# Kernel optimization log

Measured on AMD Instinct MI355X. Metric: run time of the kernel, lower is better.

## Reference

```python
import jax, jax.numpy as jnp
import numpy as np
from jax import lax

B, C, H, W = 4, 128, 256, 256
HEADS = 8
HIDDEN = int(C * 2)  # ffn_expansion_factor=2
THETA = 0.7


def _p(key, shape, scale=0.05):
    return jax.random.normal(key, shape, dtype=jnp.float32) * scale


def setup_inputs() -> dict:
    key = jax.random.key(0)
    ks = jax.random.split(key, 32)
    inp = {
        'ms': jax.random.normal(ks[0], (B, C, H, W), dtype=jnp.float32),
        'pan': jax.random.normal(ks[1], (B, C, H, W), dtype=jnp.float32),
        # LayerNorms (WithBias)
        'ln1_w': jnp.ones((C,), jnp.float32),
        'ln1_b': jnp.zeros((C,), jnp.float32),
        'ln2_w': jnp.ones((2 * C,), jnp.float32),
        'ln2_b': jnp.zeros((2 * C,), jnp.float32),
        # Attention (bias=False)
        'qkv_w': _p(ks[2], (C, C)),            # 1x1 conv weight [out,in]
        'dw_w': _p(ks[3], (C, 1, 3, 3)),       # depthwise 3x3 (Conv2d_cd)
        'temperature': jnp.ones((HEADS, 1, 1), jnp.float32),
        'proj_w': _p(ks[4], (C, C)),
        # Freprocess (default bias=True)
        'pre1_w': _p(ks[5], (C, C)), 'pre1_b': jnp.zeros((C,), jnp.float32),
        'pre2_w': _p(ks[6], (C, C)), 'pre2_b': jnp.zeros((C,), jnp.float32),
        'amp1_w': _p(ks[7], (C, 2 * C)), 'amp1_b': jnp.zeros((C,), jnp.float32),
        'amp2_w': _p(ks[8], (C, C)), 'amp2_b': jnp.zeros((C,), jnp.float32),
        'pha1_w': _p(ks[9], (C, 2 * C)), 'pha1_b': jnp.zeros((C,), jnp.float32),
        'pha2_w': _p(ks[10], (C, C)), 'pha2_b': jnp.zeros((C,), jnp.float32),
        'post_w': _p(ks[11], (C, C)), 'post_b': jnp.zeros((C,), jnp.float32),
        # FFN (bias=False)
        'pin_w': _p(ks[12], (2 * HIDDEN, 2 * C)),
        'pout_w': _p(ks[13], (C, HIDDEN)),
    }
    return inp


def conv1x1(x, w, b=None):
    y = jnp.einsum('bchw,oc->bohw', x, w)
    if b is not None:
        y = y + b[None, :, None, None]
    return y


def layernorm_c(x, w, b):
    # per-pixel LayerNorm over channel dim (torch var unbiased=False, eps=1e-5)
    mu = jnp.mean(x, axis=1, keepdims=True)
    var = jnp.mean((x - mu) ** 2, axis=1, keepdims=True)
    return (x - mu) / jnp.sqrt(var + 1e-5) * w[None, :, None, None] + b[None, :, None, None]


def dwconv_cd(x, w):
    # central-difference depthwise conv: dw3x3(x) - theta * (sum(kernel) * x)
    y = lax.conv_general_dilated(x, w, (1, 1), ((1, 1), (1, 1)),
                                 dimension_numbers=('NCHW', 'OIHW', 'NCHW'),
                                 feature_group_count=x.shape[1])
    ksum = w.sum(axis=(1, 2, 3))  # (C,)
    return y - THETA * x * ksum[None, :, None, None]


def attention(nms, npan, qkv_w, dw_w, temperature, proj_w):
    b, c, h, w = nms.shape
    ch = c // HEADS
    q = dwconv_cd(conv1x1(nms, qkv_w), dw_w)
    kv = dwconv_cd(conv1x1(npan, qkv_w), dw_w)  # k == v in source
    q = q.reshape(b, HEADS, ch, h * w)
    k = kv.reshape(b, HEADS, ch, h * w)
    v = k
    q = q / jnp.maximum(jnp.linalg.norm(q, axis=-1, keepdims=True), 1e-12)
    k = k / jnp.maximum(jnp.linalg.norm(k, axis=-1, keepdims=True), 1e-12)
    attn = jnp.einsum('bhcn,bhdn->bhcd', q, k) * temperature[None]
    attn = jax.nn.softmax(attn, axis=-1)
    out = jnp.einsum('bhcd,bhdn->bhcn', attn, v).reshape(b, c, h, w)
    return conv1x1(out, proj_w)


def freprocess(msf, panf, pre1_w, pre1_b, pre2_w, pre2_b,
               amp1_w, amp1_b, amp2_w, amp2_b,
               pha1_w, pha1_b, pha2_w, pha2_b, post_w, post_b):
    h, w = msf.shape[-2:]
    msF = jnp.fft.rfft2(conv1x1(msf, pre1_w, pre1_b) + 1e-8)
    panF = jnp.fft.rfft2(conv1x1(panf, pre2_w, pre2_b) + 1e-8)
    amp_in = jnp.concatenate([jnp.abs(msF), jnp.abs(panF)], axis=1)
    pha_in = jnp.concatenate([jnp.angle(msF), jnp.angle(panF)], axis=1)
    amp = conv1x1(jax.nn.leaky_relu(conv1x1(amp_in, amp1_w, amp1_b), 0.1), amp2_w, amp2_b)
    pha = conv1x1(jax.nn.leaky_relu(conv1x1(pha_in, pha1_w, pha1_b), 0.1), pha2_w, pha2_b)
    real = amp * jnp.cos(pha) + 1e-8
    imag = amp * jnp.sin(pha) + 1e-8
    out = jax.lax.complex(real, imag) + 1e-8
    out = jnp.abs(jnp.fft.irfft2(out, s=(h, w)))
    return conv1x1(out, post_w, post_b)


def ffn(x, pin_w, pout_w):
    y = conv1x1(x, pin_w)
    x1, x2 = jnp.split(y, 2, axis=1)
    return conv1x1(jax.nn.gelu(x1, approximate=False) * x2, pout_w)


def reference(ms, pan, ln1_w, ln1_b, ln2_w, ln2_b, qkv_w, dw_w, temperature,
              proj_w, pre1_w, pre1_b, pre2_w, pre2_b, amp1_w, amp1_b, amp2_w,
              amp2_b, pha1_w, pha1_b, pha2_w, pha2_b, post_w, post_b,
              pin_w, pout_w):
    x = ms + attention(layernorm_c(ms, ln1_w, ln1_b),
                       layernorm_c(pan, ln1_w, ln1_b),
                       qkv_w, dw_w, temperature, proj_w)
    frefuse = freprocess(ms, pan, pre1_w, pre1_b, pre2_w, pre2_b,
                         amp1_w, amp1_b, amp2_w, amp2_b,
                         pha1_w, pha1_b, pha2_w, pha2_b, post_w, post_b)
    frespa = jnp.concatenate([x, frefuse], axis=1)
    x = x + ffn(layernorm_c(frespa, ln2_w, ln2_b), pin_w, pout_w)
    return x
```

## Files before the change

kernel.cpp:

```cpp
#include <hip/hip_runtime.h>
#include <math.h>

#define B_ 4
#define C_ 128
#define HW_ 65536
#define H__ 256
#define KF_ 129
#define PLANEF_ 33024

typedef __attribute__((ext_vector_type(8))) short short8v;
typedef __attribute__((ext_vector_type(4))) float f32x4;
typedef __attribute__((ext_vector_type(4))) unsigned short ush4;
typedef __attribute__((ext_vector_type(8))) unsigned short ush8;
typedef __attribute__((ext_vector_type(4))) unsigned uint4v;

__device__ __forceinline__ unsigned short f2bf(float f) {
    union { float f; unsigned u; } v; v.f = f;
    return (unsigned short)((v.u + 0x7FFFu + ((v.u >> 16) & 1u)) >> 16);
}
__device__ __forceinline__ float bf2f(unsigned short s) {
    union { unsigned u; float f; } v; v.u = (unsigned)s << 16;
    return v.f;
}
__device__ __forceinline__ unsigned pack2bf(float2 v) {
// ... 109 lines not shown
{
    __shared__ unsigned short xs[128][136];
    __shared__ float2 lnred[LNF ? 8 : 1][LNF ? 128 : 1];
    __shared__ float2 lnmi[LNF ? 128 : 1];
    const int t = threadIdx.x;
    const int bz = blockIdx.z;
    const int p0 = blockIdx.x * 128;
    const int lane = t & 63;
    const int wr = t >> 7, wc = (t >> 6) & 1;
    const int lr = lane >> 4, lc = lane & 15;

    if constexpr (INBF == 0) {
        const float* Xb = (const float*)Xv + (size_t)bz * sx;
        const int px4 = t & 31;
        float s0 = 0.f, s1 = 0.f, s2v = 0.f, s3 = 0.f;
        float q0 = 0.f, q1 = 0.f, q2 = 0.f, q3 = 0.f;
#pragma unroll
        for (int g = 0; g < 2; ++g) {
            float4 st[8];
#pragma unroll
            for (int i = 0; i < 8; ++i) {
                int e = t + (g * 8 + i) * 256;
                int c = e >> 5;
                st[i] = *(const float4*)(Xb + (size_t)c * plane + p0 + px4 * 4);
            }
#pragma unroll
            for (int i = 0; i < 8; ++i) {
                int e = t + (g * 8 + i) * 256;
                int c = e >> 5;
                float a0 = st[i].x, a1 = st[i].y, a2 = st[i].z, a3 = st[i].w;
                if constexpr (PRO == 1) {
                    a0 = a0 > 0.f ? a0 : 0.1f * a0;
                    a1 = a1 > 0.f ? a1 : 0.1f * a1;
                    a2 = a2 > 0.f ? a2 : 0.1f * a2;
                    a3 = a3 > 0.f ? a3 : 0.1f * a3;
                }
                if constexpr (LNF) {
                    s0 += a0; q0 += a0 * a0;
                    s1 += a1; q1 += a1 * a1;
                    s2v += a2; q2 += a2 * a2;
                    s3 += a3; q3 += a3 * a3;
                }
                *(unsigned short*)swz_ptr(xs, px4 * 4 + 0, 2 * c) = f2bf(a0);
                *(unsigned short*)swz_ptr(xs, px4 * 4 + 1, 2 * c) = f2bf(a1);
                *(unsigned short*)swz_ptr(xs, px4 * 4 + 2, 2 * c) = f2bf(a2);
                *(unsigned short*)swz_ptr(xs, px4 * 4 + 3, 2 * c) = f2bf(a3);
            }
        }
        if constexpr (LNF) {
            lnred[t >> 5][px4 * 4 + 0] = make_float2(s0, q0);
            lnred[t >> 5][px4 * 4 + 1] = make_float2(s1, q1);
            lnred[t >> 5][px4 * 4 + 2] = make_float2(s2v, q2);
            lnred[t >> 5][px4 * 4 + 3] = make_float2(s3, q3);
        }
    } else {
        const unsigned short* Xb = (const unsigned short*)Xv + (size_t)bz * sx;
        ush8 st[8];
#pragma unroll
        for (int i = 0; i < 8; ++i) {
            int e = t + i * 256;
            int c = e >> 4, px8 = e & 15;
            st[i] = *(const ush8*)(Xb + (size_t)c * plane + p0 + px8 * 8);
        }
#pragma unroll
        for (int i = 0; i < 8; ++i) {
            int e = t + i * 256;
            int c = e >> 4, px8 = e & 15;
#pragma unroll
            for (int j = 0; j < 8; ++j) {
                unsigned short us = (unsigned short)st[i][j];
                if constexpr (PRO == 1) {
                    float f = bf2f(us);
                    f = f > 0.f ? f : 0.1f * f;
                    us = f2bf(f);
                }
                *(unsigned short*)swz_ptr(xs, px8 * 8 + j, 2 * c) = us;
            }
        }
    }
    __syncthreads();
    if constexpr (LNF) {
        if (t < 128) {
            float ss = 0.f, qq = 0.f;
#pragma unroll
            for (int j = 0; j < 8; ++j) { float2 a = lnred[j][t]; ss += a.x; qq += a.y; }
            float m = ss * (1.f / 128.f);
            float inv = rsqrtf(qq * (1.f / 128.f) - m * m + 1e-5f);
            lnmi[t] = make_float2(m, inv);
        }
        __syncthreads();
    }

    f32x4 acc[4][4];
#pragma unroll
    for (int mi = 0; mi < 4; ++mi)
#pragma unroll
        for (int ni = 0; ni < 4; ++ni) acc[mi][ni] = (f32x4){0.f, 0.f, 0.f, 0.f};

#pragma unroll
    for (int kk = 0; kk < 128; kk += 32) {
        short8v bfr[4];
#pragma unroll
        for (int ni = 0; ni < 4; ++ni)
            bfr[ni] = *(const short8v*)swz_ptr(xs, wc * 64 + ni * 16 + lc, 2 * (kk + lr * 8));
#pragma unroll
        for (int mi = 0; mi < 4; ++mi) {
            int row = wr * 64 + mi * 16 + lc;
            short8v afr = *(const short8v*)(Wb + (size_t)row * wstride + kk + lr * 8);
#pragma unroll
            for (int ni = 0; ni < 4; ++ni)
                acc[mi][ni] = __builtin_amdgcn_mfma_f32_16x16x32_bf16(afr, bfr[ni], acc[mi][ni], 0, 0, 0);
        }
    }

    float2 mrow[4];
    if constexpr (LNF) {
#pragma unroll
        for (int ni = 0; ni < 4; ++ni) mrow[ni] = lnmi[wc * 64 + ni * 16 + lc];
    }

#pragma unroll
    for (int mi = 0; mi < 4; ++mi) {
        int ob = wr * 64 + mi * 16 + lr * 4;
#pragma unroll
        for (int r = 0; r < 4; ++r) {
            int o = ob + r;
            float bv = 0.f, wso = 0.f;
            if constexpr (LNF) { bv = bsum[o]; wso = wsum[o]; }
            else { if (bias) bv = bias[o]; if (flags & 1) bv += 1e-8f; }
#pragma unroll
            for (int ni = 0; ni < 4; ++ni) {
                int px = wc * 64 + ni * 16 + lc;
                float v;
                if constexpr (LNF) {
                    float m = mrow[ni].x, inv = mrow[ni].y;
                    v = acc[mi][ni][r] * inv + bv - m * inv * wso;
                } else {
                    v = acc[mi][ni][r] + bv;
                }
                if constexpr (OUTBF == 0) {
                    float* Y = (float*)Yv;
                    size_t yi = (size_t)bz * sy + (size_t)o * plane + p0 + px;
                    if (res) v += res[(size_t)bz * sres + (size_t)o * plane + p0 + px];
                    Y[yi] = v;
                } else {
                    unsigned short* Y = (unsigned short*)Yv;
                    Y[(size_t)bz * sy + (size_t)o * plane + p0 + px] = f2bf(v);
                }
            }
        }
    }
}

__global__ __launch_bounds__(256, 2) void apconv2(
    const unsigned* __restrict__ T1, const unsigned* __restrict__ T2, size_t sT,
    const unsigned short* __restrict__ Wa1, const unsigned short* __restrict__ Wp1,
    const unsigned short* __restrict__ Wa2, const unsigned short* __restrict__ Wp2,
    const float* __restrict__ ba1, const float* __restrict__ bp1,
    const float* __restrict__ ba2, const float* __restrict__ bp2,
    unsigned short* __restrict__ AMP, unsigned short* __restrict__ PHA, size_t sO)
{
    __shared__ __align__(16) unsigned short buf[2][128][72];
    const int t = threadIdx.x;
    const int bz = blockIdx.z;
    const int p0 = blockIdx.x * 128;
    const int lane = t & 63;
    const int wr = t >> 7, wc = (t >> 6) & 1;
    const int lr = lane >> 4, lc = lane & 15;
    const int px2 = t & 63;

    typedef unsigned short (*row72)[72];
    typedef unsigned short (*row144)[144];
    row72 xa = (row72)buf[0];
    row72 xp = (row72)buf[1];
    row144 hb = (row144)&buf[0][0][0];

    f32x4 aa[4][4], ap[4][4];
#pragma unroll
    for (int mi = 0; mi < 4; ++mi)
#pragma unroll
        for (int ni = 0; ni < 4; ++ni) { aa[mi][ni] = (f32x4){0.f,0.f,0.f,0.f}; ap[mi][ni] = (f32x4){0.f,0.f,0.f,0.f}; }

    for (int ch = 0; ch < 256; ch += 64) {
        const unsigned* Ts = ((ch < 128) ? T1 : T2) + (size_t)bz * sT + (size_t)(ch & 127) * PLANEF_;
#pragma unroll
        for (int g = 0; g < 2; ++g) {
            uint2 st[8];
#pragma unroll
            for (int i = 0; i < 8; ++i) {
                int e = t + (g * 8 + i) * 256;
                int c = e >> 6;
                st[i] = *(const uint2*)(Ts + (size_t)c * PLANEF_ + p0 + px2 * 2);
            }
#pragma unroll
            for (int i = 0; i < 8; ++i) {
                int e = t + (g * 8 + i) * 256;
                int c = e >> 6;
                float2 z0 = upk(st[i].x), z1 = upk(st[i].y);
                float m0 = sqrtf(z0.x * z0.x + z0.y * z0.y);
                float m1 = sqrtf(z1.x * z1.x + z1.y * z1.y);
                float a0 = fatan2(z0.y, z0.x);
                float a1 = fatan2(z1.y, z1.x);
                *(unsigned short*)swz_ptr(xa, px2 * 2 + 0, 2 * c) = f2bf(m0);
                *(unsigned short*)swz_ptr(xa, px2 * 2 + 1, 2 * c) = f2bf(m1);
                *(unsigned short*)swz_ptr(xp, px2 * 2 + 0, 2 * c) = f2bf(a0);
                *(unsigned short*)swz_ptr(xp, px2 * 2 + 1, 2 * c) = f2bf(a1);
            }
        }
        __syncthreads();
#pragma unroll
        for (int kk = 0; kk < 64; kk += 32) {
            short8v bfa[4], bfp[4];
#pragma unroll
            for (int ni = 0; ni < 4; ++ni) {
                bfa[ni] = *(const short8v*)swz_ptr(xa, wc * 64 + ni * 16 + lc, 2 * (kk + lr * 8));
                bfp[ni] = *(const short8v*)swz_ptr(xp, wc * 64 + ni * 16 + lc, 2 * (kk + lr * 8));
            }
#pragma unroll
            for (int mi = 0; mi < 4; ++mi) {
                int row = wr * 64 + mi * 16 + lc;
                short8v afa = *(const short8v*)(Wa1 + (size_t)row * 256 + ch + kk + lr * 8);
                short8v afp = *(const short8v*)(Wp1 + (size_t)row * 256 + ch + kk + lr * 8);
#pragma unroll
                for (int ni = 0; ni < 4; ++ni) {
                    aa[mi][ni] = __builtin_amdgcn_mfma_f32_16x16x32_bf16(afa, bfa[ni], aa[mi][ni], 0, 0, 0);
                    ap[mi][ni] = __builtin_amdgcn_mfma_f32_16x16x32_bf16(afp, bfp[ni], ap[mi][ni], 0, 0, 0);
                }
            }
        }
        __syncthreads();
    }

#pragma unroll
    for (int mi = 0; mi < 4; ++mi)
#pragma unroll
        for (int r = 0; r < 4; ++r) {
            int o = wr * 64 + mi * 16 + lr * 4 + r;
            float bva = ba1[o];
#pragma unroll
            for (int ni = 0; ni < 4; ++ni) {
                int px = wc * 64 + ni * 16 + lc;
                float v = aa[mi][ni][r] + bva;
                v = v > 0.f ? v : 0.1f * v;
                *(unsigned short*)swz_ptr(hb, px, 2 * o) = f2bf(v);
            }
        }
    __syncthreads();
    {
        f32x4 acc[4][4];
#pragma unroll
        for (int mi = 0; mi < 4; ++mi)
#pragma unroll
            for (int ni = 0; ni < 4; ++ni) acc[mi][ni] = (f32x4){0.f,0.f,0.f,0.f};
#pragma unroll
        for (int kk = 0; kk < 128; kk += 32) {
            short8v bfr[4];
#pragma unroll
            for (int ni = 0; ni < 4; ++ni)
                bfr[ni] = *(const short8v*)swz_ptr(hb, wc * 64 + ni * 16 + lc, 2 * (kk + lr * 8));
#pragma unroll
            for (int mi = 0; mi < 4; ++mi) {
                int row = wr * 64 + mi * 16 + lc;
                short8v afr = *(const short8v*)(Wa2 + (size_t)row * 128 + kk + lr * 8);
#pragma unroll
                for (int ni = 0; ni < 4; ++ni)
                    acc[mi][ni] = __builtin_amdgcn_mfma_f32_16x16x32_bf16(afr, bfr[ni], acc[mi][ni], 0, 0, 0);
            }
        }
#pragma unroll
        for (int mi = 0; mi < 4; ++mi)
#pragma unroll
            for (int r = 0; r < 4; ++r) {
                int o = wr * 64 + mi * 16 + lr * 4 + r;
                float bv = ba2[o];
#pragma unroll
                for (int ni = 0; ni < 4; ++ni) {
                    int px = wc * 64 + ni * 16 + lc;
                    AMP[(size_t)bz * sO + (size_t)o * PLANEF_ + p0 + px] = f2bf(acc[mi][ni][r] + bv);
                }
            }
    }
    __syncthreads();

#pragma unroll
    for (int mi = 0; mi < 4; ++mi)
#pragma unroll
        for (int r = 0; r < 4; ++r) {
            int o = wr * 64 + mi * 16 + lr * 4 + r;
            float bvp = bp1[o];
#pragma unroll
            for (int ni = 0; ni < 4; ++ni) {
                int px = wc * 64 + ni * 16 + lc;
                float v = ap[mi][ni][r] + bvp;
                v = v > 0.f ? v : 0.1f * v;
                *(unsigned short*)swz_ptr(hb, px, 2 * o) = f2bf(v);
            }
        }
    __syncthreads();
    {
        f32x4 acc[4][4];
#pragma unroll
        for (int mi = 0; mi < 4; ++mi)
#pragma unroll
            for (int ni = 0; ni < 4; ++ni) acc[mi][ni] = (f32x4){0.f,0.f,0.f,0.f};
#pragma unroll
        for (int kk = 0; kk < 128; kk += 32) {
            short8v bfr[4];
#pragma unroll
            for (int ni = 0; ni < 4; ++ni)
                bfr[ni] = *(const short8v*)swz_ptr(hb, wc * 64 + ni * 16 + lc, 2 * (kk + lr * 8));
#pragma unroll
            for (int mi = 0; mi < 4; ++mi) {
                int row = wr * 64 + mi * 16 + lc;
                short8v afr = *(const short8v*)(Wp2 + (size_t)row * 128 + kk + lr * 8);
#pragma unroll
                for (int ni = 0; ni < 4; ++ni)
                    acc[mi][ni] = __builtin_amdgcn_mfma_f32_16x16x32_bf16(afr, bfr[ni], acc[mi][ni], 0, 0, 0);
            }
        }
#pragma unroll
        for (int mi = 0; mi < 4; ++mi)
#pragma unroll
            for (int r = 0; r < 4; ++r) {
                int o = wr * 64 + mi * 16 + lr * 4 + r;
                float bv = bp2[o];
#pragma unroll
                for (int ni = 0; ni < 4; ++ni) {
                    int px = wc * 64 + ni * 16 + lc;
                    PHA[(size_t)bz * sO + (size_t)o * PLANEF_ + p0 + px] = f2bf(acc[mi][ni][r] + bv);
                }
            }
    }
}

__global__ __launch_bounds__(256, 3) void ffn_mfma6(
    const float* __restrict__ x, const unsigned short* __restrict__ fre,
    const unsigned short* __restrict__ pinb,
    const unsigned short* __restrict__ pout2,
    const float4* __restrict__ pinC,
    float* __restrict__ out)
{
    __shared__ unsigned short xs[64][264];
    __shared__ unsigned short hs[64][136];
    __shared__ float2 muinv[64];
    float2* sred = (float2*)&hs[0][0];
    const int b = blockIdx.y;
    const size_t p0 = (size_t)blockIdx.x * 64;
    const int t = threadIdx.x;
    const int wave = t >> 6, lane = t & 63;
    const int lr = lane >> 4, lc = lane & 15;
    const int px4 = t & 15;

    float s0 = 0.f, s1 = 0.f, s2v = 0.f, s3 = 0.f;
    float q0 = 0.f, q1 = 0.f, q2 = 0.f, q3 = 0.f;
    {
        float4 stx[8];
        ush4 stf[8];
#pragma unroll
        for (int i = 0; i < 8; ++i) {
            int e = t + i * 256;
            int c = e >> 4;
            stx[i] = *(const float4*)(x + ((size_t)b * 128 + c) * HW_ + p0 + px4 * 4);
        }
#pragma unroll
        for (int i = 0; i < 8; ++i) {
            int e = t + i * 256;
            int c = e >> 4;
            stf[i] = *(const ush4*)(fre + (size_t)b * 8388608 + (size_t)c * HW_ + p0 + px4 * 4);
        }
#pragma unroll
        for (int i = 0; i < 8; ++i) {
            int e = t + i * 256;
            int c = e >> 4;
            float a0 = stx[i].x, a1 = stx[i].y, a2 = stx[i].z, a3 = stx[i].w;
            s0 += a0; q0 += a0 * a0;
            s1 += a1; q1 += a1 * a1;
            s2v += a2; q2 += a2 * a2;
            s3 += a3; q3 += a3 * a3;
            *(unsigned short*)swz_ptr(xs, px4 * 4 + 0, 2 * c) = f2bf(a0);
            *(unsigned short*)swz_ptr(xs, px4 * 4 + 1, 2 * c) = f2bf(a1);
            *(unsigned short*)swz_ptr(xs, px4 * 4 + 2, 2 * c) = f2bf(a2);
            *(unsigned short*)swz_ptr(xs, px4 * 4 + 3, 2 * c) = f2bf(a3);
        }
#pragma unroll
        for (int i = 0; i < 8; ++i) {
            int e = t + i * 256;
            int c = e >> 4;
            float a0 = bf2f((unsigned short)stf[i][0]);
            float a1 = bf2f((unsigned short)stf[i][1]);
            float a2 = bf2f((unsigned short)stf[i][2]);
            float a3 = bf2f((unsigned short)stf[i][3]);
            s0 += a0; q0 += a0 * a0;
            s1 += a1; q1 += a1 * a1;
            s2v += a2; q2 += a2 * a2;
            s3 += a3; q3 += a3 * a3;
            *(unsigned short*)swz_ptr(xs, px4 * 4 + 0, 2 * (128 + c)) = (unsigned short)stf[i][0];
            *(unsigned short*)swz_ptr(xs, px4 * 4 + 1, 2 * (128 + c)) = (unsigned short)stf[i][1];
            *(unsigned short*)swz_ptr(xs, px4 * 4 + 2, 2 * (128 + c)) = (unsigned short)stf[i][2];
            *(unsigned short*)swz_ptr(xs, px4 * 4 + 3, 2 * (128 + c)) = (unsigned short)stf[i][3];
        }
    }
    sred[(t >> 4) * 64 + px4 * 4 + 0] = make_float2(s0, q0);
    sred[(t >> 4) * 64 + px4 * 4 + 1] = make_float2(s1, q1);
    sred[(t >> 4) * 64 + px4 * 4 + 2] = make_float2(s2v, q2);
    sred[(t >> 4) * 64 + px4 * 4 + 3] = make_float2(s3, q3);
    __syncthreads();
    if (t < 64) {
        float ss = 0.f, qq = 0.f;
#pragma unroll
        for (int j = 0; j < 16; ++j) { float2 a = sred[j * 64 + t]; ss += a.x; qq += a.y; }
        float m = ss * (1.f / 256.f);
        float inv = rsqrtf(qq * (1.f / 256.f) - m * m + 1e-5f);
        muinv[t] = make_float2(m, inv);
    }
    __syncthreads();

    float2 mrow[4];
#pragma unroll
    for (int ni = 0; ni < 4; ++ni) mrow[ni] = muinv[ni * 16 + lc];

    f32x4 oc[2][4];
#pragma unroll
    for (int mi = 0; mi < 2; ++mi)
#pragma unroll
        for (int ni = 0; ni < 4; ++ni) oc[mi][ni] = (f32x4){0.f, 0.f, 0.f, 0.f};

#pragma unroll
    for (int half = 0; half < 2; ++half) {
        f32x4 a1[2][4], a2[2][4];
#pragma unroll
        for (int mi = 0; mi < 2; ++mi)
#pragma unroll
            for (int ni = 0; ni < 4; ++ni) { a1[mi][ni] = (f32x4){0.f,0.f,0.f,0.f}; a2[mi][ni] = (f32x4){0.f,0.f,0.f,0.f}; }

#pragma unroll
        for (int k0 = 0; k0 < 256; k0 += 32) {
            short8v bfr[4];
#pragma unroll
            for (int ni = 0; ni < 4; ++ni)
                bfr[ni] = *(const short8v*)swz_ptr(xs, ni * 16 + lc, 2 * (k0 + lr * 8));
#pragma unroll
            for (int mi = 0; mi < 2; ++mi) {
                int hrow = wave * 64 + half * 32 + mi * 16 + lc;
                short8v af1 = *(const short8v*)(pinb + (size_t)hrow * 256 + k0 + lr * 8);
                short8v af2 = *(const short8v*)(pinb + (size_t)(hrow + 256) * 256 + k0 + lr * 8);
#pragma unroll
                for (int ni = 0; ni < 4; ++ni) {
                    a1[mi][ni] = __builtin_amdgcn_mfma_f32_16x16x32_bf16(af1, bfr[ni], a1[mi][ni], 0, 0, 0);
                    a2[mi][ni] = __builtin_amdgcn_mfma_f32_16x16x32_bf16(af2, bfr[ni], a2[mi][ni], 0, 0, 0);
                }
            }
        }
        __syncthreads();
#pragma unroll
        for (int mi = 0; mi < 2; ++mi)
#pragma unroll
            for (int r = 0; r < 4; ++r) {
                int ho = wave * 64 + half * 32 + mi * 16 + lr * 4 + r;
                float4 bwc = pinC[ho];
                int kp = wave * 32 + mi * 16 + lr * 4 + r;
#pragma unroll
                for (int ni = 0; ni < 4; ++ni) {
                    float m = mrow[ni].x, inv = mrow[ni].y;
                    float v1 = a1[mi][ni][r] * inv + bwc.x - m * inv * bwc.y;
                    float v2 = a2[mi][ni][r] * inv + bwc.z - m * inv * bwc.w;
                    hs[ni * 16 + lc][kp] = f2bf(geluf(v1) * v2);
                }
            }
        __syncthreads();
#pragma unroll
        for (int k0 = 0; k0 < 128; k0 += 32) {
            short8v bfr2[4];
#pragma unroll
            for (int ni = 0; ni < 4; ++ni)
                bfr2[ni] = *(const short8v*)&hs[ni * 16 + lc][k0 + lr * 8];
#pragma unroll
            for (int mi = 0; mi < 2; ++mi) {
                int orow = wave * 32 + mi * 16 + lc;
                short8v af = *(const short8v*)(pout2 + half * 16384 + orow * 128 + k0 + lr * 8);
#pragma unroll
                for (int ni = 0; ni < 4; ++ni)
                    oc[mi][ni] = __builtin_amdgcn_mfma_f32_16x16x32_bf16(af, bfr2[ni], oc[mi][ni], 0, 0, 0);
            }
        }
    }

#pragma unroll
    for (int mi = 0; mi < 2; ++mi)
#pragma unroll
        for (int r = 0; r < 4; ++r) {
            int o = wave * 32 + mi * 16 + lr * 4 + r;
#pragma unroll
            for (int ni = 0; ni < 4; ++ni) {
                int px = ni * 16 + lc;
                float rx = bf2f(*(const unsigned short*)swz_ptr(xs, px, 2 * o));
                size_t yi = ((size_t)b * 128 + o) * HW_ + p0 + px;
                out[yi] = oc[mi][ni][r] + rx;
            }
        }
}

__global__ __launch_bounds__(256) void dwconv2(const unsigned short* __restrict__ X, size_t sx,
                                               const float* __restrict__ w9,
                                               const float* __restrict__ ksum,
                                               unsigned short* __restrict__ Y, size_t sy,
                                               float* __restrict__ ssq)
{
    int bz = blockIdx.z;
    int c = blockIdx.y;
    int p8 = blockIdx.x * 256 + threadIdx.x;
    int p0 = p8 * 8;
    int i = p0 >> 8, j0 = p0 & 255;
    const unsigned short* xp = X + (size_t)bz * sx + (size_t)c * HW_;
    const float* wc = w9 + c * 9;
    float a[8] = {0.f,0.f,0.f,0.f,0.f,0.f,0.f,0.f};
    float ctr[8];
#pragma unroll
    for (int di = -1; di <= 1; ++di) {
        int ii = i + di;
        if (ii < 0 || ii > 255) continue;
        const unsigned short* row = xp + ii * 256;
        ush8 m8 = *(const ush8*)(row + j0);
        float lft = (j0 > 0) ? bf2f(row[j0 - 1]) : 0.f;
        float rgt = (j0 < 248) ? bf2f(row[j0 + 8]) : 0.f;
        float v[10];
        v[0] = lft;
#pragma unroll
        for (int k = 0; k < 8; ++k) v[k + 1] = bf2f((unsigned short)m8[k]);
        v[9] = rgt;
        if (di == 0) {
#pragma unroll
            for (int k = 0; k < 8; ++k) ctr[k] = v[k + 1];
        }
        float w0 = wc[(di + 1) * 3], w1 = wc[(di + 1) * 3 + 1], w2 = wc[(di + 1) * 3 + 2];
#pragma unroll
        for (int k = 0; k < 8; ++k) a[k] += w0 * v[k] + w1 * v[k + 1] + w2 * v[k + 2];
    }
    float km = 0.7f * ksum[c];
    ush8 ov;
    float q = 0.f;
#pragma unroll
    for (int k = 0; k < 8; ++k) {
        float o = a[k] - km * ctr[k];
        ov[k] = f2bf(o);
        q += o * o;
    }
    *(ush8*)(Y + (size_t)bz * sy + (size_t)c * HW_ + p0) = ov;

    __shared__ float red[256];
    red[threadIdx.x] = q; __syncthreads();
    for (int st = 128; st; st >>= 1) {
        if (threadIdx.x < st) red[threadIdx.x] += red[threadIdx.x + st];
        __syncthreads();
    }
    if (!threadIdx.x) atomicAdd(&ssq[bz * C_ + c], red[0]);
}

__global__ __launch_bounds__(256) void gram_kernel(const unsigned short* __restrict__ Q, size_t sq,
                                                   const unsigned short* __restrict__ K, size_t sk,
                                                   float* __restrict__ part)
{
    int sl = blockIdx.x, h = blockIdx.y, bz = blockIdx.z;
    const unsigned short* qb = Q + (size_t)bz * sq + (size_t)(h * 16) * HW_;
    const unsigned short* kb = K + (size_t)bz * sk + (size_t)(h * 16) * HW_;
    __shared__ __align__(16) float qs[16][264];
    __shared__ __align__(16) float ks[16][264];
    int c = threadIdx.x >> 4, d = threadIdx.x & 15;
    int t = threadIdx.x;
    float acc = 0.f;
    for (int n0 = sl * 2048; n0 < (sl + 1) * 2048; n0 += 256) {
        ush4 qv[4], kv[4];
#pragma unroll
        for (int ii = 0; ii < 4; ++ii) {
            int e = t + ii * 256;
            int cc = e >> 6, n4 = e & 63;
            qv[ii] = *(const ush4*)(qb + (size_t)cc * HW_ + n0 + n4 * 4);
            kv[ii] = *(const ush4*)(kb + (size_t)cc * HW_ + n0 + n4 * 4);
        }
#pragma unroll
        for (int ii = 0; ii < 4; ++ii) {
            int e = t + ii * 256;
            int cc = e >> 6, n4 = e & 63;
#pragma unroll
            for (int j = 0; j < 4; ++j) {
                qs[cc][n4 * 4 + j] = bf2f((unsigned short)qv[ii][j]);
                ks[cc][n4 * 4 + j] = bf2f((unsigned short)kv[ii][j]);
            }
        }
        __syncthreads();
#pragma unroll 16
        for (int nn = 0; nn < 256; nn += 4) {
            float4 a4 = *(const float4*)&qs[c][nn];
            float4 b4 = *(const float4*)&ks[d][nn];
            acc += a4.x * b4.x + a4.y * b4.y + a4.z * b4.z + a4.w * b4.w;
        }
        __syncthreads();
    }
    part[((size_t)(bz * 8 + h) * 32 + sl) * 256 + threadIdx.x] = acc;
}

__global__ __launch_bounds__(256) void softmax_kernel(const float* __restrict__ part,
                                                      const float* __restrict__ nqsq,
                                                      const float* __restrict__ nksq,
                                                      const float* __restrict__ temp,
                                                      float* __restrict__ attn)
{
    int h = blockIdx.x, bz = blockIdx.y;
    int t = threadIdx.x;
    int c = t >> 4, d = t & 15;
    float g = 0.f;
    for (int sl = 0; sl < 32; ++sl) g += part[((size_t)(bz * 8 + h) * 32 + sl) * 256 + t];
    float nqv = fmaxf(sqrtf(nqsq[bz * C_ + h * 16 + c]), 1e-12f);
    float nkv = fmaxf(sqrtf(nksq[bz * C_ + h * 16 + d]), 1e-12f);
    g *= temp[h] / (nqv * nkv);
    float m = g;
#pragma unroll
    for (int off = 8; off; off >>= 1) m = fmaxf(m, __shfl_xor(m, off, 16));
    float e = __expf(g - m);
    float ssum = e;
#pragma unroll
    for (int off = 8; off; off >>= 1) ssum += __shfl_xor(ssum, off, 16);
    attn[(bz * 8 + h) * 256 + t] = e / ssum;
}

__global__ __launch_bounds__(256) void av_kernel(const float* __restrict__ attn,
                                                 const unsigned short* __restrict__ V, size_t sv,
                                                 unsigned short* __restrict__ Y, size_t sy)
{
    __shared__ __align__(16) float kv[16][260];
    __shared__ __align__(16) float at[16][16];
    int tile = blockIdx.x, h = blockIdx.y, bz = blockIdx.z;
    int n0 = tile * 256, t = threadIdx.x;
    const unsigned short* vb = V + (size_t)bz * sv + (size_t)(h * 16) * HW_;
    at[t >> 4][t & 15] = attn[(size_t)(bz * 8 + h) * 256 + (t & 15) * 16 + (t >> 4)];
#pragma unroll
    for (int i = 0; i < 4; ++i) {
        int e = t + i * 256;
        int d = e >> 6, nn4 = e & 63;
        ush4 v4 = *(const ush4*)(vb + (size_t)d * HW_ + n0 + nn4 * 4);
#pragma unroll
        for (int j = 0; j < 4; ++j) kv[d][nn4 * 4 + j] = bf2f((unsigned short)v4[j]);
    }
    __syncthreads();
    float acc[16];
#pragma unroll
    for (int cc = 0; cc < 16; ++cc) acc[cc] = 0.f;
#pragma unroll
    for (int d = 0; d < 16; ++d) {
        float kvv = kv[d][t];
        float4 a0 = *(const float4*)&at[d][0];
        float4 a1 = *(const float4*)&at[d][4];
        float4 a2 = *(const float4*)&at[d][8];
// ... 94 lines not shown
    }
#pragma unroll
    for (int ii = 0; ii < 4; ++ii) {
        int e = t + ii * 256;
        int j = e >> 6, i4 = e & 63;
#pragma unroll
        for (int q = 0; q < 4; ++q)
            sd[j][__brev((unsigned)(i4 * 4 + q)) >> 24] = upk(v4[ii][q]);
    }
    __syncthreads();
    fft_stages2(sd[t >> 5], sd[(t >> 5) + 8], tw, t & 31);
#pragma unroll
    for (int ii = 0; ii < 4; ++ii) {
        int e = t + ii * 256;
        int j = e >> 6, i4 = e & 63;
        int k = k0 + j;
        if (k < KF_) {
            uint4v o;
#pragma unroll
            for (int q = 0; q < 4; ++q) o[q] = pack2bf(sd[j][i4 * 4 + q]);
            *(uint4v*)(base + (size_t)k * 256 + i4 * 4) = o;
        }
    }
}

__global__ __launch_bounds__(256) void cifft_combine(const unsigned short* __restrict__ amp, size_t sa,
                                                     const unsigned short* __restrict__ pha, size_t sp,
                                                     unsigned* __restrict__ S, size_t ss)
{
    __shared__ float2 sd[16][256];
    __shared__ float2 tw[128];
    int t = threadIdx.x;
    int bz = blockIdx.z;
    if (t < 128) { float sn, cs; __sincosf(PI2_ * (float)t * (1.f / 256.f), &sn, &cs); tw[t] = make_float2(cs, sn); }
    int k0 = blockIdx.x * 16;
    int c = blockIdx.y;
    const unsigned short* ab = amp + (size_t)bz * sa + (size_t)c * PLANEF_;
    const unsigned short* pb = pha + (size_t)bz * sp + (size_t)c * PLANEF_;
    ush4 a4[4], p4[4];
#pragma unroll
    for (int ii = 0; ii < 4; ++ii) {
        int e = t + ii * 256;
        int j = e >> 6, i4 = e & 63;
        int k = k0 + j;
        if (k < KF_) {
            a4[ii] = *(const ush4*)(ab + (size_t)k * 256 + i4 * 4);
            p4[ii] = *(const ush4*)(pb + (size_t)k * 256 + i4 * 4);
        } else {
            a4[ii] = (ush4){0,0,0,0}; p4[ii] = (ush4){0,0,0,0};
        }
    }
#pragma unroll
    for (int ii = 0; ii < 4; ++ii) {
        int e = t + ii * 256;
        int j = e >> 6, i4 = e & 63;
        int k = k0 + j;
#pragma unroll
        for (int q = 0; q < 4; ++q) {
            float2 v = make_float2(0.f, 0.f);
            if (k < KF_) {
                float a = bf2f((unsigned short)a4[ii][q]);
                float p = bf2f((unsigned short)p4[ii][q]);
                float sn, cs;
                __sincosf(p, &sn, &cs);
                v = make_float2(a * cs + 2e-8f, a * sn + 1e-8f);
            }
            sd[j][__brev((unsigned)(i4 * 4 + q)) >> 24] = v;
        }
    }
    __syncthreads();
    fft_stages2(sd[t >> 5], sd[(t >> 5) + 8], tw, t & 31);
    unsigned* base = S + (size_t)bz * ss + (size_t)c * PLANEF_;
    for (int e = t; e < 4096; e += 256) {
        int j = e & 15, h = e >> 4;
        int k = k0 + j;
        if (k < KF_) {
            float2 o = sd[j][h];
            base[(size_t)h * KF_ + k] = pack2bf(make_float2(o.x * (1.f / 256.f), o.y * (1.f / 256.f)));
        }
    }
}

__global__ __launch_bounds__(256) void irfft_rows16_abs(const unsigned* __restrict__ S, size_t ss,
                                                        unsigned short* __restrict__ Y, size_t sy)
{
    __shared__ float2 sd[16][256];
    __shared__ float2 tw[128];
    int t = threadIdx.x;
    int bz = blockIdx.y;
    if (t < 128) { float sn, cs; __sincosf(PI2_ * (float)t * (1.f / 256.f), &sn, &cs); tw[t] = make_float2(cs, sn); }
    size_t r0 = (size_t)blockIdx.x * 16;
    const unsigned* Sb = S + (size_t)bz * ss;
    for (int e = t; e < 4096; e += 256) {
        int j = e >> 8, i = e & 255;
        const unsigned* row = Sb + (r0 + j) * 129;
        float2 v;
        if (i < 129) v = upk(row[i]);
        else { float2 w2 = upk(row[256 - i]); v = make_float2(w2.x, -w2.y); }
        sd[j][__brev((unsigned)i) >> 24] = v;
    }
    __syncthreads();
    fft_stages2(sd[t >> 5], sd[(t >> 5) + 8], tw, t & 31);
    unsigned short* Yb = Y + (size_t)bz * sy;
#pragma unroll
    for (int ii = 0; ii < 2; ++ii) {
        int e = t + ii * 256;
        int j = e >> 5, i8 = e & 31;
        ush8 ov;
#pragma unroll
        for (int q = 0; q < 8; ++q) ov[q] = f2bf(fabsf(sd[j][i8 * 8 + q].x * (1.f / 256.f)));
        *(ush8*)(Yb + (r0 + j) * 256 + i8 * 8) = ov;
    }
}

extern "C" void kernel_launch(void* const* d_in, const int* in_sizes, int n_in,
                              void* d_out, int out_size, void* d_ws, size_t ws_size,
                              hipStream_t stream)
{
    (void)in_sizes; (void)n_in; (void)out_size;
    const float* ms    = (const float*)d_in[0];
    const float* pan   = (const float*)d_in[1];
    const float* ln1w  = (const float*)d_in[2];
    const float* ln1b  = (const float*)d_in[3];
    const float* ln2w  = (const float*)d_in[4];
    const float* ln2b  = (const float*)d_in[5];
    const float* qkvw  = (const float*)d_in[6];
    const float* dww   = (const float*)d_in[7];
    const float* temp  = (const float*)d_in[8];
    const float* projw = (const float*)d_in[9];
    const float* pre1w = (const float*)d_in[10];
    const float* pre1b = (const float*)d_in[11];
    const float* pre2w = (const float*)d_in[12];
    const float* pre2b = (const float*)d_in[13];
    const float* amp1w = (const float*)d_in[14];
    const float* amp1b = (const float*)d_in[15];
    const float* amp2w = (const float*)d_in[16];
    const float* amp2b = (const float*)d_in[17];
    const float* pha1w = (const float*)d_in[18];
    const float* pha1b = (const float*)d_in[19];
    const float* pha2w = (const float*)d_in[20];
    const float* pha2b = (const float*)d_in[21];
    const float* postw = (const float*)d_in[22];
    const float* postb = (const float*)d_in[23];
    const float* pinw  = (const float*)d_in[24];
    const float* poutw = (const float*)d_in[25];

    const size_t SLOT  = 8454144;
    const size_t CHWu  = 8388608;
    const size_t CPFu  = 4227072;
    const size_t SPECu = 4227072;
    const size_t PARAMU = 344064;
    const size_t PARAMF = 273792;

    auto needB = [&](int nb) -> size_t {
        return 2ull * (33554432ull + (size_t)nb * 3ull * SLOT + PARAMU) + 4ull * PARAMF + 64;
    };
    int NB = (ws_size >= needB(4)) ? 4 : ((ws_size >= needB(2)) ? 2 : 1);

    unsigned short* F  = (unsigned short*)d_ws;
    unsigned short* U0 = F + 33554432;
    unsigned short* U1 = U0 + (size_t)NB * SLOT;
    unsigned short* U2 = U1 + (size_t)NB * SLOT;
    unsigned short* w_qkv   = U2 + (size_t)NB * SLOT;
    unsigned short* w_proj  = w_qkv  + 16384;
    unsigned short* w_pre1  = w_proj + 16384;
    unsigned short* w_pre2  = w_pre1 + 16384;
    unsigned short* w_post  = w_pre2 + 16384;
    unsigned short* w_amp1  = w_post + 16384;
    unsigned short* w_pha1  = w_amp1 + 32768;
    unsigned short* w_amp2  = w_pha1 + 32768;
    unsigned short* w_pha2  = w_amp2 + 16384;
    unsigned short* w_pin   = w_pha2 + 16384;
    unsigned short* w_pout2 = w_pin  + 131072;
    float* fpar   = (float*)(w_pout2 + 32768);
    float* ksumP  = fpar;
    float* nqsq   = ksumP + 128;
    float* nksq   = nqsq  + 512;
    float* attnP  = nksq  + 512;
    float* partP  = attnP + 8192;
    float* qkv_ws = partP + 262144;
    float* qkv_bb = qkv_ws + 128;
    float* pin_ws = qkv_bb + 128;
    float* pin_bb = pin_ws + 512;
    float* pinC   = pin_bb + 512;

    float* xout = (float*)d_out;

    auto CVT = [&](const float* src, unsigned short* dst, int n) {
        tobf16_kernel<<<(n + 255) / 256, 256, 0, stream>>>(src, dst, n);
    };
    foldln_kernel<<<128, 128, 0, stream>>>(qkvw, ln1w, ln1b, w_qkv, qkv_ws, qkv_bb, 128);
    foldln_kernel<<<512, 128, 0, stream>>>(pinw, ln2w, ln2b, w_pin, pin_ws, pin_bb, 256);
    CVT(projw, w_proj, 16384);
    CVT(pre1w, w_pre1, 16384); CVT(pre2w, w_pre2, 16384);
    CVT(postw, w_post, 16384);
    CVT(amp1w, w_amp1, 32768); CVT(pha1w, w_pha1, 32768);
    CVT(amp2w, w_amp2, 16384); CVT(pha2w, w_pha2, 16384);
    poutperm_kernel<<<128, 256, 0, stream>>>(poutw, w_pout2);
    pinc_kernel<<<1, 256, 0, stream>>>(pin_bb, pin_ws, (float4*)pinC);
    ksum_kernel<<<1, 128, 0, stream>>>(dww, ksumP);

    const size_t CHW = (size_t)C_ * HW_;
    const float* NUL = nullptr;

    for (int b0 = 0; b0 < B_; b0 += NB) {
        const float* msb  = ms  + (size_t)b0 * CHW;
        const float* panb = pan + (size_t)b0 * CHW;
        float* xb = xout + (size_t)b0 * CHW;
        unsigned short* freb = F + (size_t)b0 * CHWu;
        dim3 gz(512, 1, NB);
        dim3 gzf(258, 1, NB);

        zero2_kernel<<<(NB * 128 + 255) / 256, 256, 0, stream>>>(nqsq, nksq, NB * 128);
        mconv2<0, 1, 0, true><<<gz, 256, 0, stream>>>(
            msb, CHW, w_qkv, 128, nullptr, nullptr, 0, U0, SLOT, HW_, 0, qkv_ws, qkv_bb);
        dwconv2<<<dim3(32, 128, NB), 256, 0, stream>>>(U0, SLOT, dww, ksumP, U1, SLOT, nqsq);
        mconv2<0, 1, 0, true><<<gz, 256, 0, stream>>>(
            panb, CHW, w_qkv, 128, nullptr, nullptr, 0, U0, SLOT, HW_, 0, qkv_ws, qkv_bb);
        dwconv2<<<dim3(32, 128, NB), 256, 0, stream>>>(U0, SLOT, dww, ksumP, U2, SLOT, nksq);
        gram_kernel<<<dim3(32, 8, NB), 256, 0, stream>>>(U1, SLOT, U2, SLOT, partP);
        softmax_kernel<<<dim3(8, NB), 256, 0, stream>>>(partP, nqsq, nksq, temp, attnP);
        av_kernel<<<dim3(256, 8, NB), 256, 0, stream>>>(attnP, U2, SLOT, U0, SLOT);
        mconv2<1, 0, 0, false><<<gz, 256, 0, stream>>>(
            U0, SLOT, w_proj, 128, nullptr, msb, CHW, xb, CHW, HW_, 0, NUL, NUL);

        mconv2<0, 1, 0, false><<<gz, 256, 0, stream>>>(
            msb, CHW, w_pre1, 128, pre1b, nullptr, 0, U0, SLOT, HW_, 1, NUL, NUL);
        rfft_rowsT<<<dim3(2048, NB), 256, 0, stream>>>(U0, SLOT, (unsigned*)(void*)U1, SPECu);
        cfftT_fwd<<<dim3(9, 128, NB), 256, 0, stream>>>((unsigned*)(void*)U1, SPECu);
        mconv2<0, 1, 0, false><<<gz, 256, 0, stream>>>(
            panb, CHW, w_pre2, 128, pre2b, nullptr, 0, U0, SLOT, HW_, 1, NUL, NUL);
        rfft_rowsT<<<dim3(2048, NB), 256, 0, stream>>>(U0, SLOT, (unsigned*)(void*)U2, SPECu);
        cfftT_fwd<<<dim3(9, 128, NB), 256, 0, stream>>>((unsigned*)(void*)U2, SPECu);
        apconv2<<<gzf, 256, 0, stream>>>(
            (const unsigned*)(void*)U1, (const unsigned*)(void*)U2, SPECu,
            w_amp1, w_pha1, w_amp2, w_pha2, amp1b, pha1b, amp2b, pha2b,
            U0, U0 + CPFu, SLOT);
        cifft_combine<<<dim3(9, 128, NB), 256, 0, stream>>>(
            U0, SLOT, U0 + CPFu, SLOT, (unsigned*)(void*)U2, SPECu);
        irfft_rows16_abs<<<dim3(2048, NB), 256, 0, stream>>>((unsigned*)(void*)U2, SPECu, U0, SLOT);
        mconv2<1, 1, 0, false><<<gz, 256, 0, stream>>>(
            U0, SLOT, w_post, 128, postb, nullptr, 0, freb, CHWu, HW_, 0, NUL, NUL);
    }

    ffn_mfma6<<<dim3(HW_ / 64, B_), 256, 0, stream>>>(xout, F, w_pin, w_pout2, (const float4*)pinC, xout);
}
```

Measured before the change: 1.640 ms.

## Fuse qkv and pre 1x1 convs sharing input; stage FFN output through LDS

Adds mconv_dual, which loads each ms/pan tile once, computes the LayerNorm statistics, and runs both the qkv conv (with LN folded in) and the pre1/pre2 conv. This removes a second full read of the fp32 inputs. The extra intermediates need two more workspace slots, so a FUSED path is chosen only when the workspace is large enough, and buffer usage is reshuffled to match. The FFN epilogue now writes its results to shared memory and stores them as coalesced float4 rows instead of scattered scalar stores, at the cost of an extra barrier and LDS traffic.

```diff
diff --git a/kernel.cpp b/kernel.cpp
--- a/kernel.cpp
+++ b/kernel.cpp
@@ -285,6 +285,144 @@
     }
 }
 
+__global__ __launch_bounds__(256, 3) void mconv_dual(
+    const float* __restrict__ X, size_t sx,
+    const unsigned short* __restrict__ Wq,
+    const float* __restrict__ q_ws, const float* __restrict__ q_bb,
+    const unsigned short* __restrict__ Wp,
+    const float* __restrict__ pre_b,
+    unsigned short* __restrict__ Y1, unsigned short* __restrict__ Y2, size_t sy)
+{
+    __shared__ unsigned short xs[128][136];
+    __shared__ float2 lnred[8][128];
+    __shared__ float2 lnmi[128];
+    const int t = threadIdx.x;
+    const int bz = blockIdx.z;
+    const int p0 = blockIdx.x * 128;
+    const int lane = t & 63;
+    const int wr = t >> 7, wc = (t >> 6) & 1;
+    const int lr = lane >> 4, lc = lane & 15;
+
+    const float* Xb = X + (size_t)bz * sx;
+    const int px4 = t & 31;
+    float s0 = 0.f, s1 = 0.f, s2v = 0.f, s3 = 0.f;
+    float q0 = 0.f, q1 = 0.f, q2 = 0.f, q3 = 0.f;
+#pragma unroll
+    for (int g = 0; g < 2; ++g) {
+        float4 st[8];
+#pragma unroll
+        for (int i = 0; i < 8; ++i) {
+            int e = t + (g * 8 + i) * 256;
+            int c = e >> 5;
+            st[i] = *(const float4*)(Xb + (size_t)c * HW_ + p0 + px4 * 4);
+        }
+#pragma unroll
+        for (int i = 0; i < 8; ++i) {
+            int e = t + (g * 8 + i) * 256;
+            int c = e >> 5;
+            float a0 = st[i].x, a1 = st[i].y, a2 = st[i].z, a3 = st[i].w;
+            s0 += a0; q0 += a0 * a0;
+            s1 += a1; q1 += a1 * a1;
+            s2v += a2; q2 += a2 * a2;
+            s3 += a3; q3 += a3 * a3;
+            *(unsigned short*)swz_ptr(xs, px4 * 4 + 0, 2 * c) = f2bf(a0);
+            *(unsigned short*)swz_ptr(xs, px4 * 4 + 1, 2 * c) = f2bf(a1);
+            *(unsigned short*)swz_ptr(xs, px4 * 4 + 2, 2 * c) = f2bf(a2);
+            *(unsigned short*)swz_ptr(xs, px4 * 4 + 3, 2 * c) = f2bf(a3);
+        }
+    }
+    lnred[t >> 5][px4 * 4 + 0] = make_float2(s0, q0);
+    lnred[t >> 5][px4 * 4 + 1] = make_float2(s1, q1);
+    lnred[t >> 5][px4 * 4 + 2] = make_float2(s2v, q2);
+    lnred[t >> 5][px4 * 4 + 3] = make_float2(s3, q3);
+    __syncthreads();
+    if (t < 128) {
+        float ss = 0.f, qq = 0.f;
+#pragma unroll
+        for (int j = 0; j < 8; ++j) { float2 a = lnred[j][t]; ss += a.x; qq += a.y; }
+        float m = ss * (1.f / 128.f);
+        float inv = rsqrtf(qq * (1.f / 128.f) - m * m + 1e-5f);
+        lnmi[t] = make_float2(m, inv);
+    }
+    __syncthreads();
+
+    float2 mrow[4];
+#pragma unroll
+    for (int ni = 0; ni < 4; ++ni) mrow[ni] = lnmi[wc * 64 + ni * 16 + lc];
+
+    {
+        f32x4 acc[4][4];
+#pragma unroll
+        for (int mi = 0; mi < 4; ++mi)
+#pragma unroll
+            for (int ni = 0; ni < 4; ++ni) acc[mi][ni] = (f32x4){0.f, 0.f, 0.f, 0.f};
+#pragma unroll
+        for (int kk = 0; kk < 128; kk += 32) {
+            short8v bfr[4];
+#pragma unroll
+            for (int ni = 0; ni < 4; ++ni)
+                bfr[ni] = *(const short8v*)swz_ptr(xs, wc * 64 + ni * 16 + lc, 2 * (kk + lr * 8));
+#pragma unroll
+            for (int mi = 0; mi < 4; ++mi) {
+                int row = wr * 64 + mi * 16 + lc;
+                short8v afr = *(const short8v*)(Wq + (size_t)row * 128 + kk + lr * 8);
+#pragma unroll
+                for (int ni = 0; ni < 4; ++ni)
+                    acc[mi][ni] = __builtin_amdgcn_mfma_f32_16x16x32_bf16(afr, bfr[ni], acc[mi][ni], 0, 0, 0);
+            }
+        }
+#pragma unroll
+        for (int mi = 0; mi < 4; ++mi)
+#pragma unroll
+            for (int r = 0; r < 4; ++r) {
+                int o = wr * 64 + mi * 16 + lr * 4 + r;
+                float bv = q_bb[o], wso = q_ws[o];
+#pragma unroll
+                for (int ni = 0; ni < 4; ++ni) {
+                    int px = wc * 64 + ni * 16 + lc;
+                    float m = mrow[ni].x, inv = mrow[ni].y;
+                    float v = acc[mi][ni][r] * inv + bv - m * inv * wso;
+                    Y1[(size_t)bz * sy + (size_t)o * HW_ + p0 + px] = f2bf(v);
+                }
+            }
+    }
+
+    {
+        f32x4 acc[4][4];
+#pragma unroll
+        for (int mi = 0; mi < 4; ++mi)
+#pragma unroll
+            for (int ni = 0; ni < 4; ++ni) acc[mi][ni] = (f32x4){0.f, 0.f, 0.f, 0.f};
+#pragma unroll
+        for (int kk = 0; kk < 128; kk += 32) {
+            short8v bfr[4];
+#pragma unroll
+            for (int ni = 0; ni < 4; ++ni)
+                bfr[ni] = *(const short8v*)swz_ptr(xs, wc * 64 + ni * 16 + lc, 2 * (kk + lr * 8));
+#pragma unroll
+            for (int mi = 0; mi < 4; ++mi) {
+                int row = wr * 64 + mi * 16 + lc;
+                short8v afr = *(const short8v*)(Wp + (size_t)row * 128 + kk + lr * 8);
+#pragma unroll
+                for (int ni = 0; ni < 4; ++ni)
+                    acc[mi][ni] = __builtin_amdgcn_mfma_f32_16x16x32_bf16(afr, bfr[ni], acc[mi][ni], 0, 0, 0);
+            }
+        }
+#pragma unroll
+        for (int mi = 0; mi < 4; ++mi)
+#pragma unroll
+            for (int r = 0; r < 4; ++r) {
+                int o = wr * 64 + mi * 16 + lr * 4 + r;
+                float bv = pre_b[o] + 1e-8f;
+#pragma unroll
+                for (int ni = 0; ni < 4; ++ni) {
+                    int px = wc * 64 + ni * 16 + lc;
+                    Y2[(size_t)bz * sy + (size_t)o * HW_ + p0 + px] = f2bf(acc[mi][ni][r] + bv);
+                }
+            }
+    }
+}
+
 __global__ __launch_bounds__(256, 2) void apconv2(
     const unsigned* __restrict__ T1, const unsigned* __restrict__ T2, size_t sT,
     const unsigned short* __restrict__ Wa1, const unsigned short* __restrict__ Wp1,
@@ -466,14 +604,14 @@
     }
 }
 
-__global__ __launch_bounds__(256, 3) void ffn_mfma6(
+__global__ __launch_bounds__(256, 3) void ffn_mfma7(
     const float* __restrict__ x, const unsigned short* __restrict__ fre,
     const unsigned short* __restrict__ pinb,
     const unsigned short* __restrict__ pout2,
     const float4* __restrict__ pinC,
     float* __restrict__ out)
 {
-    __shared__ unsigned short xs[64][264];
+    __shared__ __align__(16) unsigned short xs[64][264];
     __shared__ unsigned short hs[64][136];
     __shared__ float2 muinv[64];
     float2* sred = (float2*)&hs[0][0];
@@ -618,6 +756,7 @@
         }
     }
 
+    float vout[2][4][4];
 #pragma unroll
     for (int mi = 0; mi < 2; ++mi)
 #pragma unroll
@@ -627,10 +766,30 @@
             for (int ni = 0; ni < 4; ++ni) {
                 int px = ni * 16 + lc;
                 float rx = bf2f(*(const unsigned short*)swz_ptr(xs, px, 2 * o));
-                size_t yi = ((size_t)b * 128 + o) * HW_ + p0 + px;
-                out[yi] = oc[mi][ni][r] + rx;
-            }
-        }
+                vout[mi][r][ni] = oc[mi][ni][r] + rx;
+            }
+        }
+    __syncthreads();
+    float* fb = (float*)&xs[0][0];
+#pragma unroll
+    for (int mi = 0; mi < 2; ++mi)
+#pragma unroll
+        for (int r = 0; r < 4; ++r) {
+            int o = wave * 32 + mi * 16 + lr * 4 + r;
+#pragma unroll
+            for (int ni = 0; ni < 4; ++ni)
+                fb[o * 65 + ni * 16 + lc] = vout[mi][r][ni];
+        }
+    __syncthreads();
+    float* outb = out + ((size_t)b * 128) * HW_ + p0;
+#pragma unroll
+    for (int ii = 0; ii < 8; ++ii) {
+        int e = t + ii * 256;
+        int o = e >> 4, q4 = e & 15;
+        float4 w4 = make_float4(fb[o * 65 + q4 * 4 + 0], fb[o * 65 + q4 * 4 + 1],
+                                fb[o * 65 + q4 * 4 + 2], fb[o * 65 + q4 * 4 + 3]);
+        *(float4*)(outb + (size_t)o * HW_ + q4 * 4) = w4;
+    }
 }
 
 __global__ __launch_bounds__(256) void dwconv2(const unsigned short* __restrict__ X, size_t sx,
@@ -1031,16 +1190,26 @@
     const size_t PARAMU = 344064;
     const size_t PARAMF = 273792;
 
-    auto needB = [&](int nb) -> size_t {
-        return 2ull * (33554432ull + (size_t)nb * 3ull * SLOT + PARAMU) + 4ull * PARAMF + 64;
+    auto need = [&](int nb, int nslot) -> size_t {
+        return 2ull * (33554432ull + (size_t)nb * (size_t)nslot * SLOT + PARAMU) + 4ull * PARAMF + 64;
     };
-    int NB = (ws_size >= needB(4)) ? 4 : ((ws_size >= needB(2)) ? 2 : 1);
+    int NB; bool FUSED;
+    if      (ws_size >= need(4, 5)) { NB = 4; FUSED = true;  }
+    else if (ws_size >= need(4, 3)) { NB = 4; FUSED = false; }
+    else if (ws_size >= need(2, 5)) { NB = 2; FUSED = true;  }
+    else if (ws_size >= need(2, 3)) { NB = 2; FUSED = false; }
+    else if (ws_size >= need(1, 5)) { NB = 1; FUSED = true;  }
+    else                            { NB = 1; FUSED = false; }
+    const int NSLOT = FUSED ? 5 : 3;
 
     unsigned short* F  = (unsigned short*)d_ws;
     unsigned short* U0 = F + 33554432;
     unsigned short* U1 = U0 + (size_t)NB * SLOT;
     unsigned short* U2 = U1 + (size_t)NB * SLOT;
-    unsigned short* w_qkv   = U2 + (size_t)NB * SLOT;
+    unsigned short* U3 = U2 + (size_t)NB * SLOT;
+    unsigned short* U4 = U3 + (size_t)NB * SLOT;
+    unsigned short* parU = U0 + (size_t)NB * (size_t)NSLOT * SLOT;
+    unsigned short* w_qkv   = parU;
     unsigned short* w_proj  = w_qkv  + 16384;
     unsigned short* w_pre1  = w_proj + 16384;
     unsigned short* w_pre2  = w_pre1 + 16384;
@@ -1091,36 +1260,65 @@
         dim3 gzf(258, 1, NB);
 
         zero2_kernel<<<(NB * 128 + 255) / 256, 256, 0, stream>>>(nqsq, nksq, NB * 128);
-        mconv2<0, 1, 0, true><<<gz, 256, 0, stream>>>(
-            msb, CHW, w_qkv, 128, nullptr, nullptr, 0, U0, SLOT, HW_, 0, qkv_ws, qkv_bb);
-        dwconv2<<<dim3(32, 128, NB), 256, 0, stream>>>(U0, SLOT, dww, ksumP, U1, SLOT, nqsq);
-        mconv2<0, 1, 0, true><<<gz, 256, 0, stream>>>(
-            panb, CHW, w_qkv, 128, nullptr, nullptr, 0, U0, SLOT, HW_, 0, qkv_ws, qkv_bb);
-        dwconv2<<<dim3(32, 128, NB), 256, 0, stream>>>(U0, SLOT, dww, ksumP, U2, SLOT, nksq);
-        gram_kernel<<<dim3(32, 8, NB), 256, 0, stream>>>(U1, SLOT, U2, SLOT, partP);
-        softmax_kernel<<<dim3(8, NB), 256, 0, stream>>>(partP, nqsq, nksq, temp, attnP);
-        av_kernel<<<dim3(256, 8, NB), 256, 0, stream>>>(attnP, U2, SLOT, U0, SLOT);
-        mconv2<1, 0, 0, false><<<gz, 256, 0, stream>>>(
-            U0, SLOT, w_proj, 128, nullptr, msb, CHW, xb, CHW, HW_, 0, NUL, NUL);
-
-        mconv2<0, 1, 0, false><<<gz, 256, 0, stream>>>(
-            msb, CHW, w_pre1, 128, pre1b, nullptr, 0, U0, SLOT, HW_, 1, NUL, NUL);
-        rfft_rowsT<<<dim3(2048, NB), 256, 0, stream>>>(U0, SLOT, (unsigned*)(void*)U1, SPECu);
-        cfftT_fwd<<<dim3(9, 128, NB), 256, 0, stream>>>((unsigned*)(void*)U1, SPECu);
-        mconv2<0, 1, 0, false><<<gz, 256, 0, stream>>>(
-            panb, CHW, w_pre2, 128, pre2b, nullptr, 0, U0, SLOT, HW_, 1, NUL, NUL);
-        rfft_rowsT<<<dim3(2048, NB), 256, 0, stream>>>(U0, SLOT, (unsigned*)(void*)U2, SPECu);
-        cfftT_fwd<<<dim3(9, 128, NB), 256, 0, stream>>>((unsigned*)(void*)U2, SPECu);
-        apconv2<<<gzf, 256, 0, stream>>>(
-            (const unsigned*)(void*)U1, (const unsigned*)(void*)U2, SPECu,
-            w_amp1, w_pha1, w_amp2, w_pha2, amp1b, pha1b, amp2b, pha2b,
-            U0, U0 + CPFu, SLOT);
-        cifft_combine<<<dim3(9, 128, NB), 256, 0, stream>>>(
-            U0, SLOT, U0 + CPFu, SLOT, (unsigned*)(void*)U2, SPECu);
-        irfft_rows16_abs<<<dim3(2048, NB), 256, 0, stream>>>((unsigned*)(void*)U2, SPECu, U0, SLOT);
-        mconv2<1, 1, 0, false><<<gz, 256, 0, stream>>>(
-            U0, SLOT, w_post, 128, postb, nullptr, 0, freb, CHWu, HW_, 0, NUL, NUL);
-    }
-
-    ffn_mfma6<<<dim3(HW_ / 64, B_), 256, 0, stream>>>(xout, F, w_pin, w_pout2, (const float4*)pinC, xout);
-}
+
+        if (FUSED) {
+            mconv_dual<<<gz, 256, 0, stream>>>(
+                msb, CHW, w_qkv, qkv_ws, qkv_bb, w_pre1, pre1b, U0, U1, SLOT);
+            dwconv2<<<dim3(32, 128, NB), 256, 0, stream>>>(U0, SLOT, dww, ksumP, U2, SLOT, nqsq);
+            mconv_dual<<<gz, 256, 0, stream>>>(
+                panb, CHW, w_qkv, qkv_ws, qkv_bb, w_pre2, pre2b, U0, U3, SLOT);
+            dwconv2<<<dim3(32, 128, NB), 256, 0, stream>>>(U0, SLOT, dww, ksumP, U4, SLOT, nksq);
+            gram_kernel<<<dim3(32, 8, NB), 256, 0, stream>>>(U2, SLOT, U4, SLOT, partP);
+            softmax_kernel<<<dim3(8, NB), 256, 0, stream>>>(partP, nqsq, nksq, temp, attnP);
+            av_kernel<<<dim3(256, 8, NB), 256, 0, stream>>>(attnP, U4, SLOT, U0, SLOT);
+            mconv2<1, 0, 0, false><<<gz, 256, 0, stream>>>(
+                U0, SLOT, w_proj, 128, nullptr, msb, CHW, xb, CHW, HW_, 0, NUL, NUL);
+
+            rfft_rowsT<<<dim3(2048, NB), 256, 0, stream>>>(U1, SLOT, (unsigned*)(void*)U0, SPECu);
+            cfftT_fwd<<<dim3(9, 128, NB), 256, 0, stream>>>((unsigned*)(void*)U0, SPECu);
+            rfft_rowsT<<<dim3(2048, NB), 256, 0, stream>>>(U3, SLOT, (unsigned*)(void*)U2, SPECu);
+            cfftT_fwd<<<dim3(9, 128, NB), 256, 0, stream>>>((unsigned*)(void*)U2, SPECu);
+            apconv2<<<gzf, 256, 0, stream>>>(
+                (const unsigned*)(void*)U0, (const unsigned*)(void*)U2, SPECu,
+                w_amp1, w_pha1, w_amp2, w_pha2, amp1b, pha1b, amp2b, pha2b,
+                U1, U1 + CPFu, SLOT);
+            cifft_combine<<<dim3(9, 128, NB), 256, 0, stream>>>(
+                U1, SLOT, U1 + CPFu, SLOT, (unsigned*)(void*)U3, SPECu);
+            irfft_rows16_abs<<<dim3(2048, NB), 256, 0, stream>>>((unsigned*)(void*)U3, SPECu, U0, SLOT);
+            mconv2<1, 1, 0, false><<<gz, 256, 0, stream>>>(
+                U0, SLOT, w_post, 128, postb, nullptr, 0, freb, CHWu, HW_, 0, NUL, NUL);
+        } else {
+            mconv2<0, 1, 0, true><<<gz, 256, 0, stream>>>(
+                msb, CHW, w_qkv, 128, nullptr, nullptr, 0, U0, SLOT, HW_, 0, qkv_ws, qkv_bb);
+            dwconv2<<<dim3(32, 128, NB), 256, 0, stream>>>(U0, SLOT, dww, ksumP, U1, SLOT, nqsq);
+            mconv2<0, 1, 0, true><<<gz, 256, 0, stream>>>(
+                panb, CHW, w_qkv, 128, nullptr, nullptr, 0, U0, SLOT, HW_, 0, qkv_ws, qkv_bb);
+            dwconv2<<<dim3(32, 128, NB), 256, 0, stream>>>(U0, SLOT, dww, ksumP, U2, SLOT, nksq);
+            gram_kernel<<<dim3(32, 8, NB), 256, 0, stream>>>(U1, SLOT, U2, SLOT, partP);
+            softmax_kernel<<<dim3(8, NB), 256, 0, stream>>>(partP, nqsq, nksq, temp, attnP);
+            av_kernel<<<dim3(256, 8, NB), 256, 0, stream>>>(attnP, U2, SLOT, U0, SLOT);
+            mconv2<1, 0, 0, false><<<gz, 256, 0, stream>>>(
+                U0, SLOT, w_proj, 128, nullptr, msb, CHW, xb, CHW, HW_, 0, NUL, NUL);
+
+            mconv2<0, 1, 0, false><<<gz, 256, 0, stream>>>(
+                msb, CHW, w_pre1, 128, pre1b, nullptr, 0, U0, SLOT, HW_, 1, NUL, NUL);
+            rfft_rowsT<<<dim3(2048, NB), 256, 0, stream>>>(U0, SLOT, (unsigned*)(void*)U1, SPECu);
+            cfftT_fwd<<<dim3(9, 128, NB), 256, 0, stream>>>((unsigned*)(void*)U1, SPECu);
+            mconv2<0, 1, 0, false><<<gz, 256, 0, stream>>>(
+                panb, CHW, w_pre2, 128, pre2b, nullptr, 0, U0, SLOT, HW_, 1, NUL, NUL);
+            rfft_rowsT<<<dim3(2048, NB), 256, 0, stream>>>(U0, SLOT, (unsigned*)(void*)U2, SPECu);
+            cfftT_fwd<<<dim3(9, 128, NB), 256, 0, stream>>>((unsigned*)(void*)U2, SPECu);
+            apconv2<<<gzf, 256, 0, stream>>>(
+                (const unsigned*)(void*)U1, (const unsigned*)(void*)U2, SPECu,
+                w_amp1, w_pha1, w_amp2, w_pha2, amp1b, pha1b, amp2b, pha2b,
+                U0, U0 + CPFu, SLOT);
+            cifft_combine<<<dim3(9, 128, NB), 256, 0, stream>>>(
+                U0, SLOT, U0 + CPFu, SLOT, (unsigned*)(void*)U2, SPECu);
+            irfft_rows16_abs<<<dim3(2048, NB), 256, 0, stream>>>((unsigned*)(void*)U2, SPECu, U0, SLOT);
+            mconv2<1, 1, 0, false><<<gz, 256, 0, stream>>>(
+                U0, SLOT, w_post, 128, postb, nullptr, 0, freb, CHWu, HW_, 0, NUL, NUL);
+        }
+    }
+
+    ffn_mfma7<<<dim3(HW_ / 64, B_), 256, 0, stream>>>(xout, F, w_pin, w_pout2, (const float4*)pinC, xout);
+}
```

Measured after the change: 1.608 ms. 1.02x faster.
